# Performance work log

Measured on AMD Instinct MI355X. Metric: run time of the kernel, lower is better.

Reference implementation:

```python
import jax, jax.numpy as jnp
import numpy as np
from jax import lax

B, TS, NN, FC = 16, 16, 4096, 1
HIDDEN = 64


def setup_inputs() -> dict:
    key = jax.random.key(0)
    k1, k2, k3, k4, k5 = jax.random.split(key, 5)
    x = jax.random.normal(k1, (B, TS, NN, FC), dtype=jnp.float32)
    # Conv2d(in_ch + hidden -> 4*hidden, kernel=3, padding=1), OIHW layout
    conv_w = jax.random.normal(k2, (4 * HIDDEN, FC + HIDDEN, 3, 3), dtype=jnp.float32) * 0.05
    conv_b = jax.random.normal(k3, (4 * HIDDEN,), dtype=jnp.float32) * 0.05
    # fc: Conv2d(hidden -> 1, kernel=1)
    fc_w = jax.random.normal(k4, (1, HIDDEN, 1, 1), dtype=jnp.float32) * 0.05
    fc_b = jax.random.normal(k5, (1,), dtype=jnp.float32) * 0.05
    return {"x": x, "conv_w": conv_w, "conv_b": conv_b, "fc_w": fc_w, "fc_b": fc_b}


def _convlstm_forward(x, conv_w, conv_b, fc_w, fc_b):
    Bb, Ts, Nn, Fc = x.shape
    hidden = fc_w.shape[1]
    # [B, Ts, Fc, Nn, 1] -> scan over time axis: [Ts, B, Fc, Nn, 1]
    xp = jnp.transpose(x, (0, 1, 3, 2))[..., None]
    xs = jnp.swapaxes(xp, 0, 1)
    h0 = jnp.zeros((Bb, hidden, Nn, 1), dtype=x.dtype)
    c0 = jnp.zeros_like(h0)

    dn = lax.conv_dimension_numbers(h0.shape[:1] + (Fc + hidden, Nn, 1), conv_w.shape, ("NCHW", "OIHW", "NCHW"))

    def step(carry, xt):
        h, c = carry
        inp = jnp.concatenate([xt, h], axis=1)  # [B, Fc+hidden, Nn, 1]
        gates = lax.conv_general_dilated(inp, conv_w, (1, 1), ((1, 1), (1, 1)), dimension_numbers=dn)
        gates = gates + conv_b[None, :, None, None]
        i, f, o, g = jnp.split(gates, 4, axis=1)
        c2 = jax.nn.sigmoid(f) * c + jax.nn.sigmoid(i) * jnp.tanh(g)
        h2 = jax.nn.sigmoid(o) * jnp.tanh(c2)
        return (h2, c2), None

    (h, c), _ = lax.scan(step, (h0, c0), xs)
    # fc: 1x1 conv -> [B, 1, Nn, 1]
    out = jnp.einsum("bchw,oc->bohw", h, fc_w[:, :, 0, 0]) + fc_b[None, :, None, None]
    out = out[..., 0]                 # [B, 1, Nn]
    out = jnp.transpose(out, (0, 2, 1))[:, None]  # [B, 1, Nn, 1]
    return jnp.broadcast_to(out, (Bb, Ts, Nn, 1))


def reference(x, conv_w, conv_b, fc_w, fc_b):
    return _convlstm_forward(x, conv_w, conv_b, fc_w, fc_b)
```

## Files before the change

kernel.cpp:

```cpp
#include <hip/hip_runtime.h>

typedef _Float16 f16;
typedef __attribute__((ext_vector_type(8))) _Float16 half8;
typedef __attribute__((ext_vector_type(4))) float floatx4;

#define BB    16
#define TSN   16
#define NNP   4096
#define HID   64
#define KPK   224
#define WOUT  128
#define HALO  8
#define WCMP  144
#define HROWS 146
#define NMS   9
#define NTIL  32

#define LOG2E 1.44269504088896340736f

__device__ __forceinline__ int hadr(int rr, int c) {
    return rr * 64 + ((c ^ (rr & 7)) << 3);
}
__device__ __forceinline__ unsigned f16pair(float a, float b) {
    union { f16 h; unsigned short u; } ua, ub;
    ua.h = (f16)a; ub.h = (f16)b;
    return (unsigned)ua.u | ((unsigned)ub.u << 16);
}
__device__ __forceinline__ unsigned pkrtz(float a, float b) {
    typedef __fp16 h2v __attribute__((ext_vector_type(2)));
    h2v r = __builtin_amdgcn_cvt_pkrtz(a, b);
    union { h2v h; unsigned u; } cv; cv.h = r; return cv.u;
}

__device__ __forceinline__ float fast_exp2(float x) {
#if __has_builtin(__builtin_amdgcn_exp2f)
    return __builtin_amdgcn_exp2f(x);
#else
    return exp2f(x);
#endif
}
__device__ __forceinline__ float fast_rcp(float x) {
#if __has_builtin(__builtin_amdgcn_rcpf)
    return __builtin_amdgcn_rcpf(x);
#else
    return 1.0f / x;
#endif
}

__device__ __forceinline__ float dpp_xor8(float v) {
    return __int_as_float(__builtin_amdgcn_mov_dpp(__float_as_int(v), 0x128, 0xF, 0xF, true));
}
__device__ __forceinline__ float dpp_xor1(float v) {
    return __int_as_float(__builtin_amdgcn_mov_dpp(__float_as_int(v), 0xB1, 0xF, 0xF, true));
}

__global__ void pack_w_kernel(const float* __restrict__ conv_w,
                              const float* __restrict__ conv_b,
                              f16* __restrict__ wpack) {
    int idx = blockIdx.x * 256 + threadIdx.x;
    if (idx >= 4 * 64 * KPK) return;
    int k  = idx % KPK;
    int oc = idx / KPK;
    int kt = k >> 5, c = k & 31;
    float w = 0.0f;
    if (kt < 6) {
        int tap = kt >> 1;
        int j   = (kt & 1) * 32 + c;
        w = conv_w[((oc * 65 + 1 + j) * 3 + tap) * 3 + 1];
    } else if (c < 3) {
        w = conv_w[((oc * 65 + 0) * 3 + c) * 3 + 1];
    } else if (c == 3) {
        w = conv_b[oc];
    }
    float scale = (oc >= 192) ? (2.0f * LOG2E) : (-LOG2E);
    wpack[oc * KPK + k] = (f16)(w * scale);
}

template <int MS>
__device__ __forceinline__ void do_mfx(
    const f16* __restrict__ xts, const half8 (&bf)[7][2],
    const floatx4& zacc, floatx4 (&acc)[2], int m)
{
    const int ar = MS * 16 + m;
    half8 a = *(const half8*)(xts + ar * 8);
    acc[0] = __builtin_amdgcn_mfma_f32_16x16x32_f16(a, bf[6][0], zacc, 0, 0, 0);
    acc[1] = __builtin_amdgcn_mfma_f32_16x16x32_f16(a, bf[6][1], zacc, 0, 0, 0);
}

template <int MS>
__device__ __forceinline__ void do_mfh(
    const f16* __restrict__ hrd, const half8 (&bf)[7][2],
    floatx4 (&acc)[2], int m, int kg)
{
    const int ar = MS * 16 + m;
    __builtin_amdgcn_s_setprio(1);
#pragma unroll
    for (int kt = 0; kt < 6; ++kt) {
        half8 a = *(const half8*)(hrd + hadr(ar + (kt >> 1), (kt & 1) * 4 + kg));
        acc[0] = __builtin_amdgcn_mfma_f32_16x16x32_f16(a, bf[kt][0], acc[0], 0, 0, 0);
        acc[1] = __builtin_amdgcn_mfma_f32_16x16x32_f16(a, bf[kt][1], acc[1], 0, 0, 0);
    }
    __builtin_amdgcn_s_setprio(0);
}

template <int MS>
__device__ __forceinline__ void do_epi(
    f16* __restrict__ hwr, floatx4 (&acc)[2], float (&creg)[NMS * 2],
    int m, int kg, int wave, bool lowm, bool edge, int n0)
{
    float pg[2][2];
#pragma unroll
    for (int q = 0; q < 2; ++q)
#pragma unroll
        for (int j = 0; j < 2; ++j) {
            float send = lowm ? acc[q][2 + j] : acc[q][j];
            pg[q][j] = dpp_xor8(send);
        }

    float Y[2][4];
#pragma unroll
    for (int j = 0; j < 2; ++j) {
        Y[j][0] = lowm ? acc[0][j] : pg[0][j];
        Y[j][1] = lowm ? pg[0][j] : acc[0][2 + j];
        Y[j][2] = lowm ? acc[1][j] : pg[1][j];
        Y[j][3] = lowm ? pg[1][j] : acc[1][2 + j];
    }
    float E[2][4];
#pragma unroll
    for (int j = 0; j < 2; ++j)
#pragma unroll
        for (int g = 0; g < 4; ++g) E[j][g] = fast_exp2(Y[j][g]);

#pragma unroll
    for (int j = 0; j < 2; ++j) {
        int r  = lowm ? j : 2 + j;
        float Fi = 1.0f + E[j][0], Ff = 1.0f + E[j][1];
        float Fo = 1.0f + E[j][2], Fg = 1.0f + E[j][3];
        const int ridx = MS * 2 + j;
        float P  = Fi * Fg;
        float N  = fmaf(E[j][3] - 1.0f, Ff, creg[ridx] * P);
        float cn = N * fast_rcp(P * Ff);
        float Ec = fast_exp2(cn * (2.0f * LOG2E));
        float hnf = (Ec - 1.0f) * fast_rcp(Fo * (1.0f + Ec));
        creg[ridx] = cn;
        int rit = MS * 16 + kg * 4 + r;
        if (edge) {
            int pos = n0 - HALO + rit;
            if (pos < 0 || pos >= NNP) hnf = 0.0f;
        }
        float po = dpp_xor1(hnf);
        if (!(m & 1)) {
            int rr = rit + 1;
            ((unsigned*)hwr)[rr * 32 + ((wave ^ (rr & 7)) << 2) + ((m & 7) >> 1)] =
                pkrtz(hnf, po);
        }
    }
}

__global__ __launch_bounds__(512, 2)
void lstm_kernel(const float* __restrict__ x, const f16* __restrict__ wpack,
                 f16* __restrict__ h_glob, float* __restrict__ c_glob, int phase)
{
    __shared__ __align__(16) f16 hlds[2][HROWS * 64];
    __shared__ __align__(16) f16 xt[8 * WCMP * 8];

    const int blk  = blockIdx.x;
    const int b    = blk >> 5;
    const int tau  = blk & 31;
    const int n0   = tau * WOUT;
    const int tid  = threadIdx.x;
    const int lane = tid & 63;
    const int wave = tid >> 6;
    const int m    = lane & 15;
    const int kg   = lane >> 4;
    const int gh   = m >> 3;
    const int hid  = wave * 8 + (m & 7);
    const bool lowm = (m < 8);
    const bool edge = (tau == 0) || (tau == NTIL - 1);
    const int s0   = phase * 8;

    half8 bf[7][2];
#pragma unroll
    for (int kt = 0; kt < 7; ++kt)
#pragma unroll
        for (int q = 0; q < 2; ++q)
            bf[kt][q] = *(const half8*)(wpack + (size_t)((q * 2 + gh) * 64 + hid) * KPK + kt * 32 + kg * 8);

    const floatx4 zacc = {0.0f, 0.0f, 0.0f, 0.0f};

    float creg[NMS * 2];

    for (int i = tid; i < 8 * WCMP; i += 512) {
        int ss = i / WCMP, r = i - ss * WCMP;
        const float* xb = x + ((size_t)b * TSN + s0 + ss) * NNP;
        int p = n0 - HALO + r;
        float v0 = (p - 1 >= 0 && p - 1 < NNP) ? xb[p - 1] : 0.0f;
        float v1 = (p >= 0 && p < NNP) ? xb[p] : 0.0f;
        float v2 = (p + 1 >= 0 && p + 1 < NNP) ? xb[p + 1] : 0.0f;
        unsigned* q = (unsigned*)(xt + (size_t)i * 8);
        q[0] = f16pair(v0, v1);
        q[1] = f16pair(v2, 1.0f);
        q[2] = 0u; q[3] = 0u;
    }

    if (phase == 0) {
#pragma unroll
        for (int i = 0; i < NMS * 2; ++i) creg[i] = 0.0f;
        for (int i = tid; i < HROWS * 64; i += 512) { hlds[0][i] = (f16)0; hlds[1][i] = (f16)0; }
    } else {
        for (int i = tid; i < HROWS * 8; i += 512) {
            int rr = i >> 3, c = i & 7;
            int pos = n0 - HALO - 1 + rr;
            half8 v = {};
            if (pos >= 0 && pos < NNP)
                v = *(const half8*)(h_glob + ((size_t)b * NNP + pos) * HID + c * 8);
            *(half8*)(hlds[0] + hadr(rr, c)) = v;
        }
        for (int i = tid; i < 2 * 64; i += 512) {
            int rr = (i >= 64) ? (HROWS - 1) : 0;
            hlds[1][rr * 64 + (i & 63)] = (f16)0;
        }
#pragma unroll
        for (int ms = 0; ms < NMS; ++ms)
#pragma unroll
            for (int j = 0; j < 2; ++j) {
                int r   = lowm ? j : 2 + j;
                int pos = n0 - HALO + ms * 16 + kg * 4 + r;
                creg[ms * 2 + j] = (pos >= 0 && pos < NNP)
                    ? c_glob[((size_t)b * NNP + pos) * HID + hid] : 0.0f;
            }
    }

    __syncthreads();

#pragma unroll 1
    for (int s = s0; s < s0 + 8; ++s) {
        const f16* hrd = hlds[s & 1];
        f16*       hwr = hlds[(s & 1) ^ 1];
        const f16* xts = xt + (size_t)(s - s0) * WCMP * 8;

        floatx4 accA[2], accB[2];
#define MFX(MS, A) do_mfx<MS>(xts, bf, zacc, A, m)
#define MFH(MS, A) do_mfh<MS>(hrd, bf, A, m, kg)
#define MFF(MS, A) do { MFX(MS, A); MFH(MS, A); } while (0)
#define EP(MS, A)  do_epi<MS>(hwr, A, creg, m, kg, wave, lowm, edge, n0)
        if (wave < 4) { MFX(0, accA); MFX(1, accB); }
        else          { MFX(4, accA); MFX(5, accB); }

        __syncthreads();

        if (wave < 4) {
            MFH(0, accA);
            MFH(1, accB); EP(0, accA);
            MFF(2, accA); EP(1, accB);
            MFF(3, accB); EP(2, accA);
            MFF(4, accA); EP(3, accB);
            MFF(5, accB); EP(4, accA);
            MFF(6, accA); EP(5, accB);
            MFF(7, accB); EP(6, accA);
            MFF(8, accA); EP(7, accB);
            EP(8, accA);
        } else {
            MFH(4, accA);
            MFH(5, accB); EP(4, accA);
            MFF(6, accA); EP(5, accB);
            MFF(7, accB); EP(6, accA);
            MFF(8, accA); EP(7, accB);
            MFF(0, accB); EP(8, accA);
            MFF(1, accA); EP(0, accB);
            MFF(2, accB); EP(1, accA);
            MFF(3, accA); EP(2, accB);
            EP(3, accA);
        }
#undef MFX
#undef MFH
#undef MFF
#undef EP
    }
    __syncthreads();

    for (int i = tid; i < WOUT * 8; i += 512) {
        int row = i >> 3, c = i & 7;
        half8 v = *(const half8*)(hlds[0] + hadr(row + HALO + 1, c));
        *(half8*)(h_glob + ((size_t)b * NNP + n0 + row) * HID + c * 8) = v;
    }
    if (phase == 0) {
#pragma unroll
        for (int ms = 0; ms < NMS; ++ms)
#pragma unroll
            for (int j = 0; j < 2; ++j) {
                int r   = lowm ? j : 2 + j;
                int rit = ms * 16 + kg * 4 + r;
                int pos = n0 - HALO + rit;
                if (rit >= HALO && rit < HALO + WOUT && pos >= 0 && pos < NNP)
                    c_glob[((size_t)b * NNP + pos) * HID + hid] = creg[ms * 2 + j];
            }
    }
}

__global__ void fc_kernel(const f16* __restrict__ h, const float* __restrict__ fc_w,
                          const float* __restrict__ fc_b, float* __restrict__ out) {
    int idx = blockIdx.x * 256 + threadIdx.x;
    const half8* hp = (const half8*)(h + (size_t)idx * HID);
    float s = 0.0f;
#pragma unroll
    for (int q = 0; q < 8; ++q) {
        half8 v = hp[q];
#pragma unroll
        for (int e = 0; e < 8; ++e) s += (float)v[e] * fc_w[q * 8 + e];
    }
    s += fc_b[0];
    int b = idx >> 12, n = idx & (NNP - 1);
#pragma unroll
    for (int t = 0; t < TSN; ++t) out[((size_t)b * TSN + t) * NNP + n] = s;
}

extern "C" void kernel_launch(void* const* d_in, const int* in_sizes, int n_in,
                              void* d_out, int out_size, void* d_ws, size_t ws_size,
                              hipStream_t stream) {
    const float* x      = (const float*)d_in[0];
    const float* conv_w = (const float*)d_in[1];
    const float* conv_b = (const float*)d_in[2];
    const float* fc_w   = (const float*)d_in[3];
    const float* fc_b   = (const float*)d_in[4];
    float* out = (float*)d_out;

    char* ws = (char*)d_ws;
    const size_t hbytes = (size_t)BB * NNP * HID * sizeof(f16);
    f16*   wpack  = (f16*)ws;
    f16*   h_glob = (f16*)(ws + 131072);
    float* c_glob = (float*)(ws + 131072 + hbytes);

    pack_w_kernel<<<(4 * 64 * KPK + 255) / 256, 256, 0, stream>>>(conv_w, conv_b, wpack);
    lstm_kernel<<<BB * NTIL, 512, 0, stream>>>(x, wpack, h_glob, c_glob, 0);
    lstm_kernel<<<BB * NTIL, 512, 0, stream>>>(x, wpack, h_glob, c_glob, 1);
    fc_kernel<<<BB * NNP / 256, 256, 0, stream>>>(h_glob, fc_w, fc_b, out);
}
```

Before: 254.6 us.

## Fuse both LSTM phases and the fc head into one kernel with wider halo

The halo grows from 8 to 16 rows so that each tile can run all 16 timesteps independently. This removes the mid-sequence round trip of h and c through global memory and drops the second LSTM launch. The fc 1x1 projection and the broadcast write are folded into the end of the LSTM kernel, which removes the separate fc kernel and its h read. The trade-off is about 11% more redundant recompute in the halo rows, more LDS per block, and losing the x-MFMA prefetch that previously overlapped the per-step barrier.

Result: no change. 249.8 us (-1.9%).

```diff
diff --git a/kernel.cpp b/kernel.cpp
--- a/kernel.cpp
+++ b/kernel.cpp
@@ -10,10 +10,10 @@
 #define HID   64
 #define KPK   224
 #define WOUT  128
-#define HALO  8
-#define WCMP  144
-#define HROWS 146
-#define NMS   9
+#define HALO  16
+#define WCMP  160
+#define HROWS 162
+#define NMS   10
 #define NTIL  32
 
 #define LOG2E 1.44269504088896340736f
@@ -159,7 +159,8 @@
 
 __global__ __launch_bounds__(512, 2)
 void lstm_kernel(const float* __restrict__ x, const f16* __restrict__ wpack,
-                 f16* __restrict__ h_glob, float* __restrict__ c_glob, int phase)
+                 const float* __restrict__ fc_w, const float* __restrict__ fc_b,
+                 float* __restrict__ out)
 {
     __shared__ __align__(16) f16 hlds[2][HROWS * 64];
     __shared__ __align__(16) f16 xt[8 * WCMP * 8];
@@ -177,7 +178,6 @@
     const int hid  = wave * 8 + (m & 7);
     const bool lowm = (m < 8);
     const bool edge = (tau == 0) || (tau == NTIL - 1);
-    const int s0   = phase * 8;
 
     half8 bf[7][2];
 #pragma unroll
@@ -189,69 +189,45 @@
     const floatx4 zacc = {0.0f, 0.0f, 0.0f, 0.0f};
 
     float creg[NMS * 2];
-
-    for (int i = tid; i < 8 * WCMP; i += 512) {
-        int ss = i / WCMP, r = i - ss * WCMP;
-        const float* xb = x + ((size_t)b * TSN + s0 + ss) * NNP;
-        int p = n0 - HALO + r;
-        float v0 = (p - 1 >= 0 && p - 1 < NNP) ? xb[p - 1] : 0.0f;
-        float v1 = (p >= 0 && p < NNP) ? xb[p] : 0.0f;
-        float v2 = (p + 1 >= 0 && p + 1 < NNP) ? xb[p + 1] : 0.0f;
-        unsigned* q = (unsigned*)(xt + (size_t)i * 8);
-        q[0] = f16pair(v0, v1);
-        q[1] = f16pair(v2, 1.0f);
-        q[2] = 0u; q[3] = 0u;
-    }
-
-    if (phase == 0) {
-#pragma unroll
-        for (int i = 0; i < NMS * 2; ++i) creg[i] = 0.0f;
-        for (int i = tid; i < HROWS * 64; i += 512) { hlds[0][i] = (f16)0; hlds[1][i] = (f16)0; }
-    } else {
-        for (int i = tid; i < HROWS * 8; i += 512) {
-            int rr = i >> 3, c = i & 7;
-            int pos = n0 - HALO - 1 + rr;
-            half8 v = {};
-            if (pos >= 0 && pos < NNP)
-                v = *(const half8*)(h_glob + ((size_t)b * NNP + pos) * HID + c * 8);
-            *(half8*)(hlds[0] + hadr(rr, c)) = v;
-        }
-        for (int i = tid; i < 2 * 64; i += 512) {
-            int rr = (i >= 64) ? (HROWS - 1) : 0;
-            hlds[1][rr * 64 + (i & 63)] = (f16)0;
-        }
-#pragma unroll
-        for (int ms = 0; ms < NMS; ++ms)
-#pragma unroll
-            for (int j = 0; j < 2; ++j) {
-                int r   = lowm ? j : 2 + j;
-                int pos = n0 - HALO + ms * 16 + kg * 4 + r;
-                creg[ms * 2 + j] = (pos >= 0 && pos < NNP)
-                    ? c_glob[((size_t)b * NNP + pos) * HID + hid] : 0.0f;
-            }
-    }
-
-    __syncthreads();
+#pragma unroll
+    for (int i = 0; i < NMS * 2; ++i) creg[i] = 0.0f;
+
+    auto stage_x = [&](int base) {
+        for (int i = tid; i < 8 * WCMP; i += 512) {
+            int ss = i / WCMP, r = i - ss * WCMP;
+            const float* xb = x + ((size_t)b * TSN + base + ss) * NNP;
+            int p = n0 - HALO + r;
+            float v0 = (p - 1 >= 0 && p - 1 < NNP) ? xb[p - 1] : 0.0f;
+            float v1 = (p >= 0 && p < NNP) ? xb[p] : 0.0f;
+            float v2 = (p + 1 >= 0 && p + 1 < NNP) ? xb[p + 1] : 0.0f;
+            unsigned* q = (unsigned*)(xt + (size_t)i * 8);
+            q[0] = f16pair(v0, v1);
+            q[1] = f16pair(v2, 1.0f);
+            q[2] = 0u; q[3] = 0u;
+        }
+    };
+    stage_x(0);
+
+    for (int i = tid; i < HROWS * 64; i += 512) { hlds[0][i] = (f16)0; hlds[1][i] = (f16)0; }
 
 #pragma unroll 1
-    for (int s = s0; s < s0 + 8; ++s) {
+    for (int s = 0; s < TSN; ++s) {
+        if (s == 8) {
+            __syncthreads();
+            stage_x(8);
+        }
+        __syncthreads();
+
         const f16* hrd = hlds[s & 1];
         f16*       hwr = hlds[(s & 1) ^ 1];
-        const f16* xts = xt + (size_t)(s - s0) * WCMP * 8;
+        const f16* xts = xt + (size_t)(s & 7) * WCMP * 8;
 
         floatx4 accA[2], accB[2];
-#define MFX(MS, A) do_mfx<MS>(xts, bf, zacc, A, m)
-#define MFH(MS, A) do_mfh<MS>(hrd, bf, A, m, kg)
-#define MFF(MS, A) do { MFX(MS, A); MFH(MS, A); } while (0)
+#define MFF(MS, A) do { do_mfx<MS>(xts, bf, zacc, A, m); do_mfh<MS>(hrd, bf, A, m, kg); } while (0)
 #define EP(MS, A)  do_epi<MS>(hwr, A, creg, m, kg, wave, lowm, edge, n0)
-        if (wave < 4) { MFX(0, accA); MFX(1, accB); }
-        else          { MFX(4, accA); MFX(5, accB); }
-
-        __syncthreads();
-
         if (wave < 4) {
-            MFH(0, accA);
-            MFH(1, accB); EP(0, accA);
+            MFF(0, accA);
+            MFF(1, accB); EP(0, accA);
             MFF(2, accA); EP(1, accB);
             MFF(3, accB); EP(2, accA);
             MFF(4, accA); EP(3, accB);
@@ -259,60 +235,49 @@
             MFF(6, accA); EP(5, accB);
             MFF(7, accB); EP(6, accA);
             MFF(8, accA); EP(7, accB);
-            EP(8, accA);
+            MFF(9, accB); EP(8, accA);
+            EP(9, accB);
         } else {
-            MFH(4, accA);
-            MFH(5, accB); EP(4, accA);
-            MFF(6, accA); EP(5, accB);
-            MFF(7, accB); EP(6, accA);
-            MFF(8, accA); EP(7, accB);
-            MFF(0, accB); EP(8, accA);
+            MFF(5, accA);
+            MFF(6, accB); EP(5, accA);
+            MFF(7, accA); EP(6, accB);
+            MFF(8, accB); EP(7, accA);
+            MFF(9, accA); EP(8, accB);
+            MFF(0, accB); EP(9, accA);
             MFF(1, accA); EP(0, accB);
             MFF(2, accB); EP(1, accA);
             MFF(3, accA); EP(2, accB);
-            EP(3, accA);
-        }
-#undef MFX
-#undef MFH
+            MFF(4, accB); EP(3, accA);
+            EP(4, accB);
+        }
 #undef MFF
 #undef EP
     }
     __syncthreads();
 
-    for (int i = tid; i < WOUT * 8; i += 512) {
-        int row = i >> 3, c = i & 7;
-        half8 v = *(const half8*)(hlds[0] + hadr(row + HALO + 1, c));
-        *(half8*)(h_glob + ((size_t)b * NNP + n0 + row) * HID + c * 8) = v;
-    }
-    if (phase == 0) {
-#pragma unroll
-        for (int ms = 0; ms < NMS; ++ms)
-#pragma unroll
-            for (int j = 0; j < 2; ++j) {
-                int r   = lowm ? j : 2 + j;
-                int rit = ms * 16 + kg * 4 + r;
-                int pos = n0 - HALO + rit;
-                if (rit >= HALO && rit < HALO + WOUT && pos >= 0 && pos < NNP)
-                    c_glob[((size_t)b * NNP + pos) * HID + hid] = creg[ms * 2 + j];
-            }
-    }
-}
-
-__global__ void fc_kernel(const f16* __restrict__ h, const float* __restrict__ fc_w,
-                          const float* __restrict__ fc_b, float* __restrict__ out) {
-    int idx = blockIdx.x * 256 + threadIdx.x;
-    const half8* hp = (const half8*)(h + (size_t)idx * HID);
-    float s = 0.0f;
-#pragma unroll
-    for (int q = 0; q < 8; ++q) {
-        half8 v = hp[q];
-#pragma unroll
-        for (int e = 0; e < 8; ++e) s += (float)v[e] * fc_w[q * 8 + e];
-    }
-    s += fc_b[0];
-    int b = idx >> 12, n = idx & (NNP - 1);
-#pragma unroll
-    for (int t = 0; t < TSN; ++t) out[((size_t)b * TSN + t) * NNP + n] = s;
+    {
+        const int part = tid & 3, row = tid >> 2;
+        float fw[16];
+#pragma unroll
+        for (int e = 0; e < 16; ++e) fw[e] = fc_w[part * 16 + e];
+        const int rr = row + HALO + 1;
+        float ssum = 0.0f;
+#pragma unroll
+        for (int cc = 0; cc < 2; ++cc) {
+            half8 v = *(const half8*)(hlds[0] + hadr(rr, part * 2 + cc));
+#pragma unroll
+            for (int e = 0; e < 8; ++e) ssum += (float)v[e] * fw[cc * 8 + e];
+        }
+        ssum += __shfl_xor(ssum, 1);
+        ssum += __shfl_xor(ssum, 2);
+        float* srow = (float*)xt;
+        if (part == 0) srow[row] = ssum + fc_b[0];
+        __syncthreads();
+        for (int i = tid; i < WOUT * TSN; i += 512) {
+            int tt = i >> 7, r2 = i & (WOUT - 1);
+            out[((size_t)b * TSN + tt) * NNP + n0 + r2] = srow[r2];
+        }
+    }
 }
 
 extern "C" void kernel_launch(void* const* d_in, const int* in_sizes, int n_in,
@@ -325,14 +290,8 @@
     const float* fc_b   = (const float*)d_in[4];
     float* out = (float*)d_out;
 
-    char* ws = (char*)d_ws;
-    const size_t hbytes = (size_t)BB * NNP * HID * sizeof(f16);
-    f16*   wpack  = (f16*)ws;
-    f16*   h_glob = (f16*)(ws + 131072);
-    float* c_glob = (float*)(ws + 131072 + hbytes);
+    f16* wpack = (f16*)d_ws;
 
     pack_w_kernel<<<(4 * 64 * KPK + 255) / 256, 256, 0, stream>>>(conv_w, conv_b, wpack);
-    lstm_kernel<<<BB * NTIL, 512, 0, stream>>>(x, wpack, h_glob, c_glob, 0);
-    lstm_kernel<<<BB * NTIL, 512, 0, stream>>>(x, wpack, h_glob, c_glob, 1);
-    fc_kernel<<<BB * NNP / 256, 256, 0, stream>>>(h_glob, fc_w, fc_b, out);
-}
+    lstm_kernel<<<BB * NTIL, 512, 0, stream>>>(x, wpack, fc_w, fc_b, out);
+}
```
